# Performance work log

Hardware: AMD Instinct MI355X
Metric: run time of the kernel (lower is better)

The kernel has to match this reference:

```python
import jax, jax.numpy as jnp
import numpy as np
import math

KEY_DIM = 16
COMPAT_FACTOR = 1.0 / math.sqrt(KEY_DIM)


def setup_inputs() -> dict:
    key = jax.random.key(0)
    k1, k2, k3, k4, k5 = jax.random.split(key, 5)
    B, G, D, H, K, V = 4, 2048, 128, 8, 16, 16
    h = jax.random.normal(k1, (B, G, D), dtype=jnp.float32)
    # mask: 1 = masked-out (attention forced to zero), 0 = attend
    mask = jax.random.randint(k2, (G, G), 0, 2, dtype=jnp.int32)
    # xavier_uniform over (input_dim, key_dim) fan per head
    lim_qk = math.sqrt(6.0 / (D + K))
    lim_v = math.sqrt(6.0 / (D + V))
    W_Q = jax.random.uniform(k3, (H, D, K), jnp.float32, -lim_qk, lim_qk)
    W_K = jax.random.uniform(k4, (H, D, K), jnp.float32, -lim_qk, lim_qk)
    W_V = jax.random.uniform(k5, (H, D, V), jnp.float32, -lim_v, lim_v)
    return {"h": h, "mask": mask, "W_Q": W_Q, "W_K": W_K, "W_V": W_V}


def reference(h, mask, W_Q, W_K, W_V):
    # h: [B, G, D]; W_Q/W_K: [H, D, K]; W_V: [H, D, V]; mask: [G, G] (1 = masked)
    q = jnp.einsum("bgd,hdk->bhgk", h, W_Q)  # [B, H, G, K]
    k = jnp.einsum("bgd,hdk->bhgk", h, W_K)  # [B, H, G, K]
    v = jnp.einsum("bgd,hdv->bhgv", h, W_V)  # [B, H, G, V]
    compat = COMPAT_FACTOR * jnp.einsum("bhqk,bhgk->bhqg", q, k)  # [B, H, G, G]
    masked = (mask > 0)[None, None, :, :]  # broadcast over batch, heads
    neg = jnp.finfo(compat.dtype).min
    compat = jnp.where(masked, neg, compat)
    attn = jax.nn.softmax(compat, axis=-1)
    # post-softmax hard zeroing at masked positions (as in the original)
    attn = jnp.where(masked, jnp.zeros((), attn.dtype), attn)
    h_p = jnp.einsum("bhqg,bhgv->bhqv", attn, v)  # [B, H, G, V]
    return h_p
```

## Files before the change

### kernel.cpp

```cpp
#include <hip/hip_runtime.h>
#include <hip/hip_bf16.h>

#define GG 2048
#define DD 128
#define HH 8
#define BH 32

typedef _Float16 h2 __attribute__((ext_vector_type(2)));
typedef _Float16 h4 __attribute__((ext_vector_type(4)));
typedef _Float16 h8 __attribute__((ext_vector_type(8)));
typedef __attribute__((ext_vector_type(4))) float f32x4;
typedef unsigned short u16;
typedef unsigned int   u32;
typedef unsigned char  u8;
typedef unsigned long long u64;

#define QSCALE 0.36067376022224085f

#define OFF_Q  0u
#define OFF_KV (2u << 20)
#define OFF_M  (6u << 20)

#if __has_builtin(__builtin_amdgcn_exp2f)
#define EXP2F(x) __builtin_amdgcn_exp2f(x)
#else
#define EXP2F(x) exp2f(x)
#endif

#define MFMA16(a, b, c) __builtin_amdgcn_mfma_f32_16x16x16f16(a, b, c, 0, 0, 0)

static __device__ __forceinline__ u16 f16b(float x) {
  return __builtin_bit_cast(u16, (_Float16)x);
}

__global__ __launch_bounds__(256) void prep_kernel(
    const float* __restrict__ h, const int* __restrict__ mask,
    const float* __restrict__ WQ, const float* __restrict__ WK,
    const float* __restrict__ WV,
    _Float16* __restrict__ Qh, u8* __restrict__ KVp, u8* __restrict__ mbt)
{
  const int blk = blockIdx.x, tid = threadIdx.x;

  if (blk >= 256) {
    int t = (blk - 256) * 256 + tid;
    const int* m = mask + (size_t)t * 8;
    int4 m0 = *(const int4*)m;
    int4 m1 = *(const int4*)(m + 4);
    u32 byte = (m0.x > 0) | ((m0.y > 0) << 1) | ((m0.z > 0) << 2) | ((m0.w > 0) << 3)
             | ((m1.x > 0) << 4) | ((m1.y > 0) << 5) | ((m1.z > 0) << 6) | ((m1.w > 0) << 7);
    int q  = t >> 8;
    int k8 = t & 255;
    mbt[(size_t)(k8 >> 4) * (GG * 16) + (size_t)q * 16 + (k8 & 15)] = (u8)byte;
    return;
  }

  __shared__ _Float16 Wl[48 * 136];
  const int bh = blk >> 3, b = bh >> 3, hh = bh & (HH - 1);

  #pragma unroll
  for (int m = 0; m < 3; ++m) {
    const float* W = (m == 0 ? WQ : (m == 1 ? WK : WV)) + (size_t)hh * DD * 16;
    const float sc = (m == 0) ? QSCALE : 1.0f;
    #pragma unroll
    for (int i = 0; i < 2; ++i) {
      int j4 = i * 256 + tid;
      float4 v = ((const float4*)W)[j4];
      int j = j4 * 4, d = j >> 4, n0 = m * 16 + (j & 15);
      Wl[(n0 + 0) * 136 + d] = (_Float16)(v.x * sc);
      Wl[(n0 + 1) * 136 + d] = (_Float16)(v.y * sc);
      Wl[(n0 + 2) * 136 + d] = (_Float16)(v.z * sc);
      Wl[(n0 + 3) * 136 + d] = (_Float16)(v.w * sc);
    }
  }
  __syncthreads();

  const int wave = tid >> 6, lane = tid & 63;
  const int col = lane & 15, quad = lane >> 4;
  const int g0 = ((blk & 7) * 4 + wave) * 64;
  const float* hb = h + (size_t)b * GG * DD;

  f32x4 acc[4][3];
  #pragma unroll
  for (int mt = 0; mt < 4; ++mt)
    #pragma unroll
    for (int nt = 0; nt < 3; ++nt)
      acc[mt][nt] = (f32x4){0.f, 0.f, 0.f, 0.f};

  #pragma unroll
  for (int s = 0; s < 4; ++s) {
    h8 a[4], bw[3];
    #pragma unroll
    for (int mt = 0; mt < 4; ++mt) {
      const float* src = hb + (size_t)(g0 + mt * 16 + col) * DD + s * 32 + quad * 8;
      float4 x = ((const float4*)src)[0];
      float4 y = ((const float4*)src)[1];
      a[mt] = (h8){ (_Float16)x.x, (_Float16)x.y, (_Float16)x.z, (_Float16)x.w,
                    (_Float16)y.x, (_Float16)y.y, (_Float16)y.z, (_Float16)y.w };
    }
    #pragma unroll
    for (int nt = 0; nt < 3; ++nt)
      bw[nt] = *(const h8*)&Wl[(nt * 16 + col) * 136 + s * 32 + quad * 8];
    #pragma unroll
    for (int mt = 0; mt < 4; ++mt)
      #pragma unroll
      for (int nt = 0; nt < 3; ++nt)
        acc[mt][nt] = __builtin_amdgcn_mfma_f32_16x16x32_f16(a[mt], bw[nt], acc[mt][nt], 0, 0, 0);
  }

  u8* kvb = KVp + (size_t)bh * 16 * 8192;
  #pragma unroll
  for (int mt = 0; mt < 4; ++mt) {
    #pragma unroll
    for (int r = 0; r < 4; ++r) {
      int g = g0 + mt * 16 + quad * 4 + r;
      Qh[((size_t)bh * GG + g) * 16 + col] = (_Float16)acc[mt][0][r];
      int gi = g & 127;
      u8* tb = kvb + (size_t)(g >> 7) * 8192;
      *(u16*)(tb + gi * 32 + col * 2) = f16b(acc[mt][1][r]);
      *(u16*)(tb + 4096 + col * 256 + ((((gi >> 2) + col) & 31) * 8)
                 + (g & 3) * 2) = f16b(acc[mt][2][r]);
    }
  }
}

__global__ __launch_bounds__(1024, 8) void attn_kernel(
    const _Float16* __restrict__ Qh, const u8* __restrict__ KVp,
    const u8* __restrict__ mbt, float* __restrict__ out)
{
  __shared__ __align__(16) u8 kv[2][16384];
  __shared__ float Lacc[8][16][17];
  __shared__ float Ll[8][16];
  __shared__ __align__(16) f32x4 cmLUT[16];
  const int tid = threadIdx.x, wv = tid >> 6, lane = tid & 63;
  const int col = lane & 15, quad = lane >> 4;
  const int qt = wv & 7;
  const int kh = wv >> 3;
  const int bh = blockIdx.x & 31;
  const int qb = (blockIdx.x >> 5) * 128 + qt * 16;

  if (tid < 16) {
    f32x4 e;
    e[0] = (tid & 1) ? -3000.f : -4.f;
    e[1] = (tid & 2) ? -3000.f : -4.f;
    e[2] = (tid & 4) ? -3000.f : -4.f;
    e[3] = (tid & 8) ? -3000.f : -4.f;
    cmLUT[tid] = e;
  }

  const h4 qf = *(const h4*)(Qh + ((size_t)bh * GG + qb + col) * 16 + quad * 4);
  const u8* kvsrc = KVp + (size_t)bh * 16 * 8192;
  const u8* mrow  = mbt + (size_t)(qb + col) * 16;

  f32x4 acc = {0.f,0.f,0.f,0.f}, lacc = {0.f,0.f,0.f,0.f};
  const h4 ones = {(_Float16)1.f, (_Float16)1.f, (_Float16)1.f, (_Float16)1.f};
  const int shq = quad * 4;

  const int sh2 = tid >> 9, stid = tid & 511;

  *(uint4*)(kv[0] + sh2 * 8192 + stid * 16) =
      *(const uint4*)(kvsrc + (size_t)(sh2 * 8) * 8192 + stid * 16);
  const size_t tstep = (size_t)(GG * 16);
  uint4 mv = *(const uint4*)(mrow + (size_t)(kh * 8) * tstep);
  __syncthreads();

  for (int it = 0; it < 8; ++it) {
    uint4 ns, nm;
    if (it < 7) {
      ns = *(const uint4*)(kvsrc + (size_t)(sh2 * 8 + it + 1) * 8192 + stid * 16);
      nm = *(const uint4*)(mrow + (size_t)(kh * 8 + it + 1) * tstep);
    }

    const u8* cur = kv[it & 1] + kh * 8192;
    const _Float16* ldsK = (const _Float16*)cur;
    const u8* ldsV = cur + 4096;
    u64 w0 = ((u64)mv.x | ((u64)mv.y << 32)) >> shq;
    u64 w1 = ((u64)mv.z | ((u64)mv.w << 32)) >> shq;

    #pragma unroll
    for (int st = 0; st < 8; ++st) {
      h4 kf = *(const h4*)(ldsK + (size_t)(st * 16 + col) * 16 + quad * 4);
      h4 vf = *(const h4*)(ldsV + col * 256 + (((st * 4 + quad + col) & 31) * 8));

      u32 bits = (u32)(((st < 4) ? w0 : w1) >> ((st & 3) * 16)) & 0xFu;
      const f32x4 cm = cmLUT[bits];

      f32x4 s = MFMA16(kf, qf, cm);
      float p0 = EXP2F(s[0]);
      float p1 = EXP2F(s[1]);
      float p2 = EXP2F(s[2]);
      float p3 = EXP2F(s[3]);

      h2 a01 = __builtin_bit_cast(h2, __builtin_amdgcn_cvt_pkrtz(p0, p1));
      h2 a23 = __builtin_bit_cast(h2, __builtin_amdgcn_cvt_pkrtz(p2, p3));
      h4 pf = __builtin_shufflevector(a01, a23, 0, 1, 2, 3);

      acc  = MFMA16(vf, pf, acc);
      lacc = MFMA16(ones, pf, lacc);
    }

    if (it < 7) {
      *(uint4*)(kv[(it + 1) & 1] + sh2 * 8192 + stid * 16) = ns;
      mv = nm;
      __syncthreads();
    }
  }

  const float l = lacc[0];
  if (kh == 0) {
    #pragma unroll
    for (int r = 0; r < 4; ++r) Lacc[qt][col][shq + r] = acc[r];
    if (quad == 0) Ll[qt][col] = l;
  }
  __syncthreads();
  if (kh == 1) {
    float la = Ll[qt][col] + l;
    float ra = (la > 0.f) ? (1.f / la) : 0.f;
    float4 o;
    o.x = (Lacc[qt][col][shq + 0] + acc[0]) * ra;
    o.y = (Lacc[qt][col][shq + 1] + acc[1]) * ra;
    o.z = (Lacc[qt][col][shq + 2] + acc[2]) * ra;
    o.w = (Lacc[qt][col][shq + 3] + acc[3]) * ra;
    *(float4*)(out + ((size_t)bh * GG + qb + col) * 16 + shq) = o;
  }
}

extern "C" void kernel_launch(void* const* d_in, const int* in_sizes, int n_in,
                              void* d_out, int out_size, void* d_ws, size_t ws_size,
                              hipStream_t stream) {
  const float* h    = (const float*)d_in[0];
  const int*   mask = (const int*)d_in[1];
  const float* WQ   = (const float*)d_in[2];
  const float* WK   = (const float*)d_in[3];
  const float* WV   = (const float*)d_in[4];
  float* out = (float*)d_out;
  char* ws = (char*)d_ws;
  _Float16* Qh  = (_Float16*)(ws + OFF_Q);
  u8*       KVp = (u8*)(ws + OFF_KV);
  u8*       mbt = (u8*)(ws + OFF_M);

  hipLaunchKernelGGL(prep_kernel, dim3(256 + GG * GG / (256 * 8)), dim3(256), 0, stream,
                     h, mask, WQ, WK, WV, Qh, KVp, mbt);
  hipLaunchKernelGGL(attn_kernel, dim3(BH * (GG / 128)), dim3(1024), 0, stream,
                     Qh, KVp, mbt, out);
}
```

Measured before the change: 106.0 us.

## Process two query tiles per wave so K/V LDS fragments are reused

Attention blocks shrink from 16 to 8 waves, and each wave now handles two 16-row query tiles. Each K and V fragment read from LDS therefore feeds two sets of MFMAs, halving LDS read traffic per unit of work. V-fragment LDS offsets are precomputed per step. In exchange each wave holds more registers and there are fewer waves to hide latency, and each thread does twice the global-to-LDS staging loads.

```diff
diff --git a/kernel.cpp b/kernel.cpp
--- a/kernel.cpp
+++ b/kernel.cpp
@@ -123,7 +123,7 @@
   }
 }
 
-__global__ __launch_bounds__(1024, 8) void attn_kernel(
+__global__ __launch_bounds__(512, 4) void attn_kernel(
     const _Float16* __restrict__ Qh, const u8* __restrict__ KVp,
     const u8* __restrict__ mbt, float* __restrict__ out)
 {
@@ -133,10 +133,12 @@
   __shared__ __align__(16) f32x4 cmLUT[16];
   const int tid = threadIdx.x, wv = tid >> 6, lane = tid & 63;
   const int col = lane & 15, quad = lane >> 4;
-  const int qt = wv & 7;
-  const int kh = wv >> 3;
+  const int qp = wv & 3;
+  const int kh = wv >> 2;
   const int bh = blockIdx.x & 31;
-  const int qb = (blockIdx.x >> 5) * 128 + qt * 16;
+  const int qt0 = qp * 2, qt1 = qp * 2 + 1;
+  const int qb0 = (blockIdx.x >> 5) * 128 + qt0 * 16;
+  const int qb1 = qb0 + 16;
 
   if (tid < 16) {
     f32x4 e;
@@ -147,80 +149,123 @@
     cmLUT[tid] = e;
   }
 
-  const h4 qf = *(const h4*)(Qh + ((size_t)bh * GG + qb + col) * 16 + quad * 4);
+  const h4 qf0 = *(const h4*)(Qh + ((size_t)bh * GG + qb0 + col) * 16 + quad * 4);
+  const h4 qf1 = *(const h4*)(Qh + ((size_t)bh * GG + qb1 + col) * 16 + quad * 4);
   const u8* kvsrc = KVp + (size_t)bh * 16 * 8192;
-  const u8* mrow  = mbt + (size_t)(qb + col) * 16;
-
-  f32x4 acc = {0.f,0.f,0.f,0.f}, lacc = {0.f,0.f,0.f,0.f};
+  const u8* mrow0 = mbt + (size_t)(qb0 + col) * 16;
+  const u8* mrow1 = mbt + (size_t)(qb1 + col) * 16;
+
+  f32x4 acc0 = {0.f,0.f,0.f,0.f}, lacc0 = {0.f,0.f,0.f,0.f};
+  f32x4 acc1 = {0.f,0.f,0.f,0.f}, lacc1 = {0.f,0.f,0.f,0.f};
   const h4 ones = {(_Float16)1.f, (_Float16)1.f, (_Float16)1.f, (_Float16)1.f};
   const int shq = quad * 4;
 
-  const int sh2 = tid >> 9, stid = tid & 511;
-
-  *(uint4*)(kv[0] + sh2 * 8192 + stid * 16) =
-      *(const uint4*)(kvsrc + (size_t)(sh2 * 8) * 8192 + stid * 16);
+  int voff[8];
+  #pragma unroll
+  for (int st = 0; st < 8; ++st)
+    voff[st] = kh * 8192 + 4096 + col * 256 + (((st * 4 + quad + col) & 31) * 8);
+  const int koff = kh * 8192;
+
+  const int sh2 = tid >> 8, stid = tid & 255;
+
+  {
+    const u8* src = kvsrc + (size_t)(sh2 * 8) * 8192;
+    *(uint4*)(kv[0] + sh2 * 8192 + stid * 16)        = *(const uint4*)(src + stid * 16);
+    *(uint4*)(kv[0] + sh2 * 8192 + 4096 + stid * 16) = *(const uint4*)(src + 4096 + stid * 16);
+  }
   const size_t tstep = (size_t)(GG * 16);
-  uint4 mv = *(const uint4*)(mrow + (size_t)(kh * 8) * tstep);
+  uint4 mv0 = *(const uint4*)(mrow0 + (size_t)(kh * 8) * tstep);
+  uint4 mv1 = *(const uint4*)(mrow1 + (size_t)(kh * 8) * tstep);
   __syncthreads();
 
   for (int it = 0; it < 8; ++it) {
-    uint4 ns, nm;
+    uint4 ns0, ns1, nm0, nm1;
     if (it < 7) {
-      ns = *(const uint4*)(kvsrc + (size_t)(sh2 * 8 + it + 1) * 8192 + stid * 16);
-      nm = *(const uint4*)(mrow + (size_t)(kh * 8 + it + 1) * tstep);
-    }
-
-    const u8* cur = kv[it & 1] + kh * 8192;
-    const _Float16* ldsK = (const _Float16*)cur;
-    const u8* ldsV = cur + 4096;
-    u64 w0 = ((u64)mv.x | ((u64)mv.y << 32)) >> shq;
-    u64 w1 = ((u64)mv.z | ((u64)mv.w << 32)) >> shq;
+      const u8* src = kvsrc + (size_t)(sh2 * 8 + it + 1) * 8192;
+      ns0 = *(const uint4*)(src + stid * 16);
+      ns1 = *(const uint4*)(src + 4096 + stid * 16);
+      nm0 = *(const uint4*)(mrow0 + (size_t)(kh * 8 + it + 1) * tstep);
+      nm1 = *(const uint4*)(mrow1 + (size_t)(kh * 8 + it + 1) * tstep);
+    }
+
+    const u8* cur = kv[it & 1];
+    const _Float16* ldsK = (const _Float16*)(cur + koff);
+    u64 a0 = ((u64)mv0.x | ((u64)mv0.y << 32)) >> shq;
+    u64 a1 = ((u64)mv0.z | ((u64)mv0.w << 32)) >> shq;
+    u64 b0 = ((u64)mv1.x | ((u64)mv1.y << 32)) >> shq;
+    u64 b1 = ((u64)mv1.z | ((u64)mv1.w << 32)) >> shq;
 
     #pragma unroll
     for (int st = 0; st < 8; ++st) {
       h4 kf = *(const h4*)(ldsK + (size_t)(st * 16 + col) * 16 + quad * 4);
-      h4 vf = *(const h4*)(ldsV + col * 256 + (((st * 4 + quad + col) & 31) * 8));
-
-      u32 bits = (u32)(((st < 4) ? w0 : w1) >> ((st & 3) * 16)) & 0xFu;
-      const f32x4 cm = cmLUT[bits];
-
-      f32x4 s = MFMA16(kf, qf, cm);
-      float p0 = EXP2F(s[0]);
-      float p1 = EXP2F(s[1]);
-      float p2 = EXP2F(s[2]);
-      float p3 = EXP2F(s[3]);
+      h4 vf = *(const h4*)(cur + voff[st]);
+
+      u32 bitsA = (u32)(((st < 4) ? a0 : a1) >> ((st & 3) * 16)) & 0xFu;
+      u32 bitsB = (u32)(((st < 4) ? b0 : b1) >> ((st & 3) * 16)) & 0xFu;
+      const f32x4 cmA = cmLUT[bitsA];
+      const f32x4 cmB = cmLUT[bitsB];
+
+      f32x4 s0 = MFMA16(kf, qf0, cmA);
+      f32x4 s1 = MFMA16(kf, qf1, cmB);
+      float p0 = EXP2F(s0[0]);
+      float p1 = EXP2F(s0[1]);
+      float p2 = EXP2F(s0[2]);
+      float p3 = EXP2F(s0[3]);
+      float r0 = EXP2F(s1[0]);
+      float r1 = EXP2F(s1[1]);
+      float r2 = EXP2F(s1[2]);
+      float r3 = EXP2F(s1[3]);
 
       h2 a01 = __builtin_bit_cast(h2, __builtin_amdgcn_cvt_pkrtz(p0, p1));
       h2 a23 = __builtin_bit_cast(h2, __builtin_amdgcn_cvt_pkrtz(p2, p3));
-      h4 pf = __builtin_shufflevector(a01, a23, 0, 1, 2, 3);
-
-      acc  = MFMA16(vf, pf, acc);
-      lacc = MFMA16(ones, pf, lacc);
+      h4 pf0 = __builtin_shufflevector(a01, a23, 0, 1, 2, 3);
+      h2 c01 = __builtin_bit_cast(h2, __builtin_amdgcn_cvt_pkrtz(r0, r1));
+      h2 c23 = __builtin_bit_cast(h2, __builtin_amdgcn_cvt_pkrtz(r2, r3));
+      h4 pf1 = __builtin_shufflevector(c01, c23, 0, 1, 2, 3);
+
+      acc0  = MFMA16(vf, pf0, acc0);
+      acc1  = MFMA16(vf, pf1, acc1);
+      lacc0 = MFMA16(ones, pf0, lacc0);
+      lacc1 = MFMA16(ones, pf1, lacc1);
     }
 
     if (it < 7) {
-      *(uint4*)(kv[(it + 1) & 1] + sh2 * 8192 + stid * 16) = ns;
-      mv = nm;
+      u8* dst = kv[(it + 1) & 1] + sh2 * 8192;
+      *(uint4*)(dst + stid * 16)        = ns0;
+      *(uint4*)(dst + 4096 + stid * 16) = ns1;
+      mv0 = nm0; mv1 = nm1;
       __syncthreads();
     }
   }
 
-  const float l = lacc[0];
+  const float l0 = lacc0[0], l1 = lacc1[0];
   if (kh == 0) {
     #pragma unroll
-    for (int r = 0; r < 4; ++r) Lacc[qt][col][shq + r] = acc[r];
-    if (quad == 0) Ll[qt][col] = l;
+    for (int r = 0; r < 4; ++r) {
+      Lacc[qt0][col][shq + r] = acc0[r];
+      Lacc[qt1][col][shq + r] = acc1[r];
+    }
+    if (quad == 0) { Ll[qt0][col] = l0; Ll[qt1][col] = l1; }
   }
   __syncthreads();
   if (kh == 1) {
-    float la = Ll[qt][col] + l;
-    float ra = (la > 0.f) ? (1.f / la) : 0.f;
-    float4 o;
-    o.x = (Lacc[qt][col][shq + 0] + acc[0]) * ra;
-    o.y = (Lacc[qt][col][shq + 1] + acc[1]) * ra;
-    o.z = (Lacc[qt][col][shq + 2] + acc[2]) * ra;
-    o.w = (Lacc[qt][col][shq + 3] + acc[3]) * ra;
-    *(float4*)(out + ((size_t)bh * GG + qb + col) * 16 + shq) = o;
+    float la0 = Ll[qt0][col] + l0;
+    float ra0 = (la0 > 0.f) ? (1.f / la0) : 0.f;
+    float4 o0;
+    o0.x = (Lacc[qt0][col][shq + 0] + acc0[0]) * ra0;
+    o0.y = (Lacc[qt0][col][shq + 1] + acc0[1]) * ra0;
+    o0.z = (Lacc[qt0][col][shq + 2] + acc0[2]) * ra0;
+    o0.w = (Lacc[qt0][col][shq + 3] + acc0[3]) * ra0;
+    *(float4*)(out + ((size_t)bh * GG + qb0 + col) * 16 + shq) = o0;
+
+    float la1 = Ll[qt1][col] + l1;
+    float ra1 = (la1 > 0.f) ? (1.f / la1) : 0.f;
+    float4 o1;
+    o1.x = (Lacc[qt1][col][shq + 0] + acc1[0]) * ra1;
+    o1.y = (Lacc[qt1][col][shq + 1] + acc1[1]) * ra1;
+    o1.z = (Lacc[qt1][col][shq + 2] + acc1[2]) * ra1;
+    o1.w = (Lacc[qt1][col][shq + 3] + acc1[3]) * ra1;
+    *(float4*)(out + ((size_t)bh * GG + qb1 + col) * 16 + shq) = o1;
   }
 }
 
@@ -240,6 +285,6 @@
 
   hipLaunchKernelGGL(prep_kernel, dim3(256 + GG * GG / (256 * 8)), dim3(256), 0, stream,
                      h, mask, WQ, WK, WV, Qh, KVp, mbt);
-  hipLaunchKernelGGL(attn_kernel, dim3(BH * (GG / 128)), dim3(1024), 0, stream,
+  hipLaunchKernelGGL(attn_kernel, dim3(BH * (GG / 128)), dim3(512), 0, stream,
                      Qh, KVp, mbt, out);
 }
```

After: 103.3 us. 1.03x faster.
